# Optimization experiments

Measured on AMD Instinct MI355X. Metric: run time of the kernel, lower is better.

## Reference

```python
import jax, jax.numpy as jnp
import numpy as np

# Hyper-parameters (defaults of EnergyHyperParameters)
BETA = 1.0
ALPHA = 1.0
LAMBDA_L2 = 0.01
LAMBDA_SMOOTH = 0.001  # unused: compute_grad defaults to False so grad_z is None


def setup_inputs() -> dict:
    key = jax.random.key(0)
    k1, k2, k3 = jax.random.split(key, 3)
    B, N, D = 4096, 65536, 256
    z = jax.random.normal(k1, (B, D), dtype=jnp.float32)
    z_next = jax.random.normal(k2, (B, D), dtype=jnp.float32)
    memory_patterns = jax.random.normal(k3, (N, D), dtype=jnp.float32)
    return {"z": z, "z_next": z_next, "memory_patterns": memory_patterns}


def reference(z, z_next, memory_patterns):
    # Hopfield energy: -logsumexp(beta * z @ M^T) per row, then mean
    logits = BETA * jnp.einsum("bd,nd->bn", z, memory_patterns)  # [B, N]
    hopfield = jnp.mean(-jax.nn.logsumexp(logits, axis=-1))
    # DEQ consistency: alpha * mean ||z - z_next||^2
    consistency = ALPHA * jnp.mean(jnp.sum((z - z_next) ** 2, axis=-1))
    # Regularization: lambda_l2 * mean ||z||^2 (no smoothness term, grad_z is None)
    regularization = LAMBDA_L2 * jnp.mean(jnp.sum(z * z, axis=-1))
    total = hopfield + consistency + regularization
    return (total, hopfield, consistency, regularization)
```

## Files before the change

### kernel.cpp

```cpp
#include <hip/hip_runtime.h>
#include <stdint.h>


typedef __attribute__((ext_vector_type(8))) int   v8i;
typedef __attribute__((ext_vector_type(4))) float f32x4;

#define N_PAT  65536
#define D_DIM  256
#define B_ROWS 4096
#define NSPLIT 16
#define NRANGE (N_PAT / NSPLIT)
#define SPR    (NRANGE / 16)
#define SPERW  (SPR / 2)
#define BBLK   128
#define SHIFT2 69.0f
#define LOG2E  1.44269504f
#define LN2    0.69314718f
#define SCL1   0x7F7F7F7F

#define WS_M_OFF   ((size_t)0)
#define WS_M_BYTES ((size_t)N_PAT * D_DIM)
#define WS_Z_OFF   (WS_M_OFF + WS_M_BYTES)
#define WS_Z_BYTES ((size_t)B_ROWS * D_DIM)
#define WS_LSE_OFF (WS_Z_OFF + WS_Z_BYTES)
#define WS_LSE_BYTES ((size_t)B_ROWS * NSPLIT * 2 * 4)
#define WS_CSS_OFF (WS_LSE_OFF + WS_LSE_BYTES)
#define WS_ZSS_OFF (WS_CSS_OFF + (size_t)512 * 4)

__device__ __forceinline__ float fexp2(float x) {
  return __builtin_amdgcn_exp2f(x);
}

__device__ __forceinline__ int pk4_fp8(float a, float b, float c, float d) {
  int r = __builtin_amdgcn_cvt_pk_fp8_f32(a, b, 0, false);
  r = __builtin_amdgcn_cvt_pk_fp8_f32(c, d, r, true);
  return r;
}

__device__ __forceinline__ float waveRedAdd(float v) {
  #pragma unroll
  for (int o = 32; o > 0; o >>= 1) v += __shfl_down(v, o, 64);
  return v;
}

__global__ void convert_m_kernel(const float* __restrict__ src, int* __restrict__ dst) {
  const int c = blockIdx.x * 256 + threadIdx.x;
  const int row = c >> 5;
  const int j = c & 31;
  const float* sp = src + (size_t)row * D_DIM + j * 8;
  const float4 x = *(const float4*)(sp);
  const float4 y = *(const float4*)(sp + 4);
  int2 o;
  o.x = pk4_fp8(x.x, x.y, x.z, x.w);
  o.y = pk4_fp8(y.x, y.y, y.z, y.w);
  const size_t dw = (size_t)(row >> 4) * 1024 + (j >> 4) * 512 +
                    (((j >> 2) & 3) * 16 + (row & 15)) * 8 + (j & 3) * 2;
  *(int2*)(dst + dw) = o;
}

__global__ void prep_z_kernel(const float* __restrict__ z, const float* __restrict__ zn,
                              int* __restrict__ z8, float* __restrict__ css,
                              float* __restrict__ zss) {
  int t = blockIdx.x * 256 + threadIdx.x;
  const float* az = z + (size_t)t * 8;
  const float* an = zn + (size_t)t * 8;
  float4 z0 = *(const float4*)(az), z1 = *(const float4*)(az + 4);
  float4 n0 = *(const float4*)(an), n1 = *(const float4*)(an + 4);
  float zv[8] = {z0.x, z0.y, z0.z, z0.w, z1.x, z1.y, z1.z, z1.w};
  float nv[8] = {n0.x, n0.y, n0.z, n0.w, n1.x, n1.y, n1.z, n1.w};
  float cs = 0.f, zs = 0.f;
  #pragma unroll
  for (int j = 0; j < 8; ++j) {
    float d = zv[j] - nv[j];
    cs += d * d;
    zs += zv[j] * zv[j];
  }
  int2 o;
  o.x = pk4_fp8(zv[0] * LOG2E, zv[1] * LOG2E, zv[2] * LOG2E, zv[3] * LOG2E);
  o.y = pk4_fp8(zv[4] * LOG2E, zv[5] * LOG2E, zv[6] * LOG2E, zv[7] * LOG2E);
  *(int2*)(z8 + (size_t)t * 2) = o;

  __shared__ float rc[4], rz[4];
  cs = waveRedAdd(cs);
  zs = waveRedAdd(zs);
  int w = threadIdx.x >> 6, lane = threadIdx.x & 63;
  if (lane == 0) { rc[w] = cs; rz[w] = zs; }
  __syncthreads();
  if (threadIdx.x == 0) {
    css[blockIdx.x] = rc[0] + rc[1] + rc[2] + rc[3];
    zss[blockIdx.x] = rz[0] + rz[1] + rz[2] + rz[3];
  }
}

__global__ __launch_bounds__(256, 2) void lse_kernel(const int* __restrict__ Mp,
                                                     const int* __restrict__ z8,
                                                     float* __restrict__ lsep) {
  const int bid = blockIdx.x;
  const int xcd = bid & 7;
  const int g = bid >> 3;
  const int bblk = g & 31;
  const int half = g >> 5;
  const int nsplit = xcd * 2 + half;

  const int tid = threadIdx.x;
  const int w = tid >> 6;
  const int lane = tid & 63;
  const int l15 = lane & 15;
  const int grp = lane >> 4;
  const int bh = w & 1;
  const int nh = w >> 1;

  if (half) __builtin_amdgcn_s_sleep(5);

  v8i zf[4][2];
  const int brow0 = bblk * BBLK + bh * 64;
  #pragma unroll
  for (int bt = 0; bt < 4; ++bt) {
    #pragma unroll
    for (int kh = 0; kh < 2; ++kh) {
      int row = brow0 + bt * 16 + l15;
      zf[bt][kh] = *(const v8i*)(z8 + (size_t)row * 64 + kh * 32 + grp * 8);
    }
  }

  const int* pj = Mp + (size_t)(nsplit * SPR + nh) * 1024 + lane * 8;

  float ssum[4] = {0.f, 0.f, 0.f, 0.f};
  f32x4 accA[4], accB[4];
  v8i afA[2], afB[2];

  #pragma unroll
  for (int bt = 0; bt < 4; ++bt)
    #pragma unroll
    for (int q = 0; q < 4; ++q) accB[bt][q] = -INFINITY;

  #pragma unroll
  for (int kh = 0; kh < 2; ++kh) afA[kh] = *(const v8i*)(pj + kh * 512);

  auto body = [&](f32x4 (&CUR)[4], f32x4 (&PREV)[4], v8i (&CURF)[2], v8i (&NXTF)[2]) {
    const int* pn = pj + 2048;
    #pragma unroll
    for (int kh = 0; kh < 2; ++kh) NXTF[kh] = *(const v8i*)(pn + kh * 512);

    #pragma unroll
    for (int bt = 0; bt < 4; ++bt)
      #pragma unroll
      for (int q = 0; q < 4; ++q) CUR[bt][q] = -SHIFT2;

    __builtin_amdgcn_s_setprio(1);
    #pragma unroll
    for (int kh = 0; kh < 2; ++kh)
      #pragma unroll
      for (int bt = 0; bt < 4; ++bt)
        CUR[bt] = __builtin_amdgcn_mfma_scale_f32_16x16x128_f8f6f4(
            CURF[kh], zf[bt][kh], CUR[bt], 0, 0, 0, SCL1, 0, SCL1);
    __builtin_amdgcn_s_setprio(0);

    #pragma unroll
    for (int bt = 0; bt < 4; ++bt)
      ssum[bt] += (fexp2(PREV[bt][0]) + fexp2(PREV[bt][1])) +
                  (fexp2(PREV[bt][2]) + fexp2(PREV[bt][3]));

    pj = pn;
  };

  #pragma unroll 1
  for (int jp = 0; jp < SPERW / 2; ++jp) {
    body(accA, accB, afA, afB);
    body(accB, accA, afB, afA);
  }

  #pragma unroll
  for (int bt = 0; bt < 4; ++bt)
    ssum[bt] += (fexp2(accB[bt][0]) + fexp2(accB[bt][1])) +
                (fexp2(accB[bt][2]) + fexp2(accB[bt][3]));

  #pragma unroll
  for (int bt = 0; bt < 4; ++bt) {
    ssum[bt] += __shfl_xor(ssum[bt], 16, 64);
    ssum[bt] += __shfl_xor(ssum[bt], 32, 64);
  }
  if (grp == 0) {
    #pragma unroll
    for (int bt = 0; bt < 4; ++bt) {
      int b = brow0 + bt * 16 + l15;
      lsep[(size_t)b * (NSPLIT * 2) + nsplit * 2 + nh] = ssum[bt];
    }
  }
}

__global__ void finalize_kernel(const float* __restrict__ lsep, const float* __restrict__ css,
                                const float* __restrict__ zss, float* __restrict__ out) {
  __shared__ float r1[16], r2[16], r3[16];
  int tid = threadIdx.x;
  float sum_lse = 0.f;
  for (int r = tid; r < B_ROWS; r += 1024) {
    float S = 0.f;
    #pragma unroll
    for (int i = 0; i < NSPLIT * 2; ++i) S += lsep[(size_t)r * (NSPLIT * 2) + i];
    sum_lse += SHIFT2 * LN2 + logf(S);
  }
  float cs = 0.f, zs = 0.f;
  if (tid < 512) { cs = css[tid]; zs = zss[tid]; }

  sum_lse = waveRedAdd(sum_lse);
  cs = waveRedAdd(cs);
  zs = waveRedAdd(zs);
  int w = tid >> 6, lane = tid & 63;
  if (lane == 0) { r1[w] = sum_lse; r2[w] = cs; r3[w] = zs; }
  __syncthreads();
  if (tid == 0) {
    float sl = 0.f, sc = 0.f, sz = 0.f;
    #pragma unroll
    for (int i = 0; i < 16; ++i) { sl += r1[i]; sc += r2[i]; sz += r3[i]; }
    float hop = -sl / (float)B_ROWS;
    float cons = sc / (float)B_ROWS;
    float reg = 0.01f * sz / (float)B_ROWS;
    out[0] = hop + cons + reg;
    out[1] = hop;
    out[2] = cons;
    out[3] = reg;
  }
}

extern "C" void kernel_launch(void* const* d_in, const int* in_sizes, int n_in,
                              void* d_out, int out_size, void* d_ws, size_t ws_size,
                              hipStream_t stream) {
  (void)in_sizes; (void)n_in; (void)out_size; (void)ws_size;
  const float* z  = (const float*)d_in[0];
  const float* zn = (const float*)d_in[1];
  const float* M  = (const float*)d_in[2];
  char* ws = (char*)d_ws;
  int* Mp  = (int*)(ws + WS_M_OFF);
  int* z8  = (int*)(ws + WS_Z_OFF);
  float* lsep = (float*)(ws + WS_LSE_OFF);
  float* css = (float*)(ws + WS_CSS_OFF);
  float* zss = (float*)(ws + WS_ZSS_OFF);

  convert_m_kernel<<<8192, 256, 0, stream>>>(M, Mp);
  prep_z_kernel<<<512, 256, 0, stream>>>(z, zn, z8, css, zss);
  lse_kernel<<<512, 256, 0, stream>>>(Mp, z8, lsep);
  finalize_kernel<<<1, 1024, 0, stream>>>(lsep, css, zss, (float*)d_out);
}
```

Baseline: 95.45 us.

## Split N range four ways per block and double grid with higher occupancy

The LSE kernel now has each of the four waves cover a distinct 64-row slice of a 256-row B block. Each block processes a quarter of its N sub-range instead of waves splitting N in halves. The grid doubles to 1024 blocks, launch bounds rise to 4 blocks per SM, and the partial-sum buffer and finalize loop widen to 64 partitions. The explicit ping-pong software pipelining (MFMA of one tile overlapped with exp of the previous) and the staggered sleep are removed. The kernel now relies on more resident waves to hide latency, at the cost of per-wave ILP and of holding the register budget under 4-way occupancy.

Measured after the change: 119.7 us. 25.4% more time.

```diff
diff --git a/kernel.cpp b/kernel.cpp
--- a/kernel.cpp
+++ b/kernel.cpp
@@ -11,8 +11,9 @@
 #define NSPLIT 16
 #define NRANGE (N_PAT / NSPLIT)
 #define SPR    (NRANGE / 16)
-#define SPERW  (SPR / 2)
-#define BBLK   128
+#define SPERW4 (SPR / 4)
+#define BBLK   256
+#define NPART  (NSPLIT * 4)
 #define SHIFT2 69.0f
 #define LOG2E  1.44269504f
 #define LN2    0.69314718f
@@ -23,7 +24,7 @@
 #define WS_Z_OFF   (WS_M_OFF + WS_M_BYTES)
 #define WS_Z_BYTES ((size_t)B_ROWS * D_DIM)
 #define WS_LSE_OFF (WS_Z_OFF + WS_Z_BYTES)
-#define WS_LSE_BYTES ((size_t)B_ROWS * NSPLIT * 2 * 4)
+#define WS_LSE_BYTES ((size_t)B_ROWS * NPART * 4)
 #define WS_CSS_OFF (WS_LSE_OFF + WS_LSE_BYTES)
 #define WS_ZSS_OFF (WS_CSS_OFF + (size_t)512 * 4)
 
@@ -92,28 +93,26 @@
   }
 }
 
-__global__ __launch_bounds__(256, 2) void lse_kernel(const int* __restrict__ Mp,
+__global__ __launch_bounds__(256, 4) void lse_kernel(const int* __restrict__ Mp,
                                                      const int* __restrict__ z8,
                                                      float* __restrict__ lsep) {
   const int bid = blockIdx.x;
   const int xcd = bid & 7;
   const int g = bid >> 3;
-  const int bblk = g & 31;
-  const int half = g >> 5;
+  const int half = g >> 6;
   const int nsplit = xcd * 2 + half;
+  const int rem = g & 63;
+  const int bblk = rem & 15;
+  const int q = rem >> 4;
 
   const int tid = threadIdx.x;
   const int w = tid >> 6;
   const int lane = tid & 63;
   const int l15 = lane & 15;
   const int grp = lane >> 4;
-  const int bh = w & 1;
-  const int nh = w >> 1;
-
-  if (half) __builtin_amdgcn_s_sleep(5);
 
   v8i zf[4][2];
-  const int brow0 = bblk * BBLK + bh * 64;
+  const int brow0 = bblk * BBLK + w * 64;
   #pragma unroll
   for (int bt = 0; bt < 4; ++bt) {
     #pragma unroll
@@ -123,57 +122,41 @@
     }
   }
 
-  const int* pj = Mp + (size_t)(nsplit * SPR + nh) * 1024 + lane * 8;
-
+  const int* pj = Mp + (size_t)(nsplit * SPR + q) * 1024 + lane * 8;
+
+  const f32x4 INITC = {-SHIFT2, -SHIFT2, -SHIFT2, -SHIFT2};
   float ssum[4] = {0.f, 0.f, 0.f, 0.f};
-  f32x4 accA[4], accB[4];
-  v8i afA[2], afB[2];
-
-  #pragma unroll
-  for (int bt = 0; bt < 4; ++bt)
-    #pragma unroll
-    for (int q = 0; q < 4; ++q) accB[bt][q] = -INFINITY;
-
-  #pragma unroll
-  for (int kh = 0; kh < 2; ++kh) afA[kh] = *(const v8i*)(pj + kh * 512);
-
-  auto body = [&](f32x4 (&CUR)[4], f32x4 (&PREV)[4], v8i (&CURF)[2], v8i (&NXTF)[2]) {
-    const int* pn = pj + 2048;
-    #pragma unroll
-    for (int kh = 0; kh < 2; ++kh) NXTF[kh] = *(const v8i*)(pn + kh * 512);
-
+  f32x4 acc[4];
+  v8i af[2];
+
+  #pragma unroll
+  for (int kh = 0; kh < 2; ++kh) af[kh] = *(const v8i*)(pj + kh * 512);
+
+  #pragma unroll 1
+  for (int j = 0; j < SPERW4; ++j) {
+    const int* pn = pj + 4096;
+
+    __builtin_amdgcn_s_setprio(1);
     #pragma unroll
     for (int bt = 0; bt < 4; ++bt)
-      #pragma unroll
-      for (int q = 0; q < 4; ++q) CUR[bt][q] = -SHIFT2;
-
-    __builtin_amdgcn_s_setprio(1);
-    #pragma unroll
-    for (int kh = 0; kh < 2; ++kh)
-      #pragma unroll
-      for (int bt = 0; bt < 4; ++bt)
-        CUR[bt] = __builtin_amdgcn_mfma_scale_f32_16x16x128_f8f6f4(
-            CURF[kh], zf[bt][kh], CUR[bt], 0, 0, 0, SCL1, 0, SCL1);
+      acc[bt] = __builtin_amdgcn_mfma_scale_f32_16x16x128_f8f6f4(
+          af[0], zf[bt][0], INITC, 0, 0, 0, SCL1, 0, SCL1);
+    #pragma unroll
+    for (int bt = 0; bt < 4; ++bt)
+      acc[bt] = __builtin_amdgcn_mfma_scale_f32_16x16x128_f8f6f4(
+          af[1], zf[bt][1], acc[bt], 0, 0, 0, SCL1, 0, SCL1);
     __builtin_amdgcn_s_setprio(0);
 
     #pragma unroll
+    for (int kh = 0; kh < 2; ++kh) af[kh] = *(const v8i*)(pn + kh * 512);
+
+    #pragma unroll
     for (int bt = 0; bt < 4; ++bt)
-      ssum[bt] += (fexp2(PREV[bt][0]) + fexp2(PREV[bt][1])) +
-                  (fexp2(PREV[bt][2]) + fexp2(PREV[bt][3]));
+      ssum[bt] += (fexp2(acc[bt][0]) + fexp2(acc[bt][1])) +
+                  (fexp2(acc[bt][2]) + fexp2(acc[bt][3]));
 
     pj = pn;
-  };
-
-  #pragma unroll 1
-  for (int jp = 0; jp < SPERW / 2; ++jp) {
-    body(accA, accB, afA, afB);
-    body(accB, accA, afB, afA);
-  }
-
-  #pragma unroll
-  for (int bt = 0; bt < 4; ++bt)
-    ssum[bt] += (fexp2(accB[bt][0]) + fexp2(accB[bt][1])) +
-                (fexp2(accB[bt][2]) + fexp2(accB[bt][3]));
+  }
 
   #pragma unroll
   for (int bt = 0; bt < 4; ++bt) {
@@ -184,7 +167,7 @@
     #pragma unroll
     for (int bt = 0; bt < 4; ++bt) {
       int b = brow0 + bt * 16 + l15;
-      lsep[(size_t)b * (NSPLIT * 2) + nsplit * 2 + nh] = ssum[bt];
+      lsep[(size_t)b * NPART + nsplit * 4 + q] = ssum[bt];
     }
   }
 }
@@ -197,7 +180,7 @@
   for (int r = tid; r < B_ROWS; r += 1024) {
     float S = 0.f;
     #pragma unroll
-    for (int i = 0; i < NSPLIT * 2; ++i) S += lsep[(size_t)r * (NSPLIT * 2) + i];
+    for (int i = 0; i < NPART; ++i) S += lsep[(size_t)r * NPART + i];
     sum_lse += SHIFT2 * LN2 + logf(S);
   }
   float cs = 0.f, zs = 0.f;
@@ -239,6 +222,6 @@
 
   convert_m_kernel<<<8192, 256, 0, stream>>>(M, Mp);
   prep_z_kernel<<<512, 256, 0, stream>>>(z, zn, z8, css, zss);
-  lse_kernel<<<512, 256, 0, stream>>>(Mp, z8, lsep);
+  lse_kernel<<<1024, 256, 0, stream>>>(Mp, z8, lsep);
   finalize_kernel<<<1, 1024, 0, stream>>>(lsep, css, zss, (float*)d_out);
 }
```
